# Optimization experiments

Measured on AMD Instinct MI355X. Metric: run time of the kernel, lower is better.

## Reference

```python
import jax, jax.numpy as jnp
import numpy as np

TEMPERATURE = 1.0
NUM_EXPERTS = 8


def setup_inputs() -> dict:
    key = jax.random.key(0)
    ks = jax.random.split(key, 7)
    B, S, H, E = 4, 4096, 1024, NUM_EXPERTS
    scale = 1.0 / np.sqrt(H)
    return {
        "hidden_states": jax.random.normal(ks[0], (B, S, H), dtype=jnp.float32),
        "w1": jax.random.normal(ks[1], (H, H // 2), dtype=jnp.float32) * scale,
        "b1": jax.random.normal(ks[2], (H // 2,), dtype=jnp.float32) * 0.01,
        "w2": jax.random.normal(ks[3], (H // 2, E), dtype=jnp.float32) * (1.0 / np.sqrt(H // 2)),
        "b2": jax.random.normal(ks[4], (E,), dtype=jnp.float32) * 0.01,
        "expert_W": jax.random.normal(ks[5], (E, H, H), dtype=jnp.float32) * scale,
        "expert_b": jax.random.normal(ks[6], (E, H), dtype=jnp.float32) * 0.01,
    }


def reference(hidden_states, w1, b1, w2, b2, expert_W, expert_b):
    # Router MLP: Linear(H, H//2) -> ReLU -> Linear(H//2, E)  (dropout inactive at eval)
    h = jax.nn.relu(jnp.einsum("bsh,hm->bsm", hidden_states, w1) + b1)
    routing_scores = (jnp.einsum("bsm,me->bse", h, w2) + b2) / TEMPERATURE
    expert_probs = jax.nn.softmax(routing_scores, axis=-1)
    # top-1 routing (topk with k=1 == argmax of probs)
    top_idx = jnp.argmax(expert_probs, axis=-1)  # [B, S]
    onehot = jax.nn.one_hot(top_idx, NUM_EXPERTS, dtype=hidden_states.dtype)  # [B, S, E]

    # _apply_expert_routing: for each expert, masked input -> dense transform -> masked accumulate
    routed = jnp.zeros_like(hidden_states)
    for e in range(NUM_EXPERTS):
        mask = onehot[..., e:e + 1]  # [B, S, 1]
        expert_out = jnp.einsum("bsh,hd->bsd", hidden_states * mask, expert_W[e]) + expert_b[e]
        routed = routed + expert_out * mask
    return routed
```

## Files before the change

### kernel.cpp

```cpp
#include <hip/hip_runtime.h>

#define NTOK 16384
#define HDIM 1024
#define MDIM 512
#define NEXP 8
#define CHUNK 128
#define MAXCHUNK 136
#define RCAP 4096
#define DELTA 0.02f
#define LSTR 72

#define G1_NWG ((MDIM / 128) * (NTOK / 128))
#define EG_NWG (8 * MAXCHUNK)

#define PREP_CVT 8192
#define PREP_W1 128
#define PREP_EW 2048
#define PREP_TOTAL (PREP_CVT + PREP_W1 + PREP_EW + 1)

typedef __bf16 bf16x8 __attribute__((ext_vector_type(8)));
typedef float floatx4 __attribute__((ext_vector_type(4)));

__device__ __forceinline__ void gll16(const void* g, void* l) {
  __builtin_amdgcn_global_load_lds(
      (const __attribute__((address_space(1))) void*)g,
      (__attribute__((address_space(3))) void*)l, 16, 0, 0);
}

__global__ __launch_bounds__(256) void prep(
    const float* __restrict__ hs, __bf16* __restrict__ hs_bf,
    const float* __restrict__ w1, __bf16* __restrict__ w1t,
    const float* __restrict__ eW, __bf16* __restrict__ eWt,
    int* __restrict__ ctrl, int* __restrict__ fillm1)
{
  __shared__ __align__(16) __bf16 T[64 * LSTR];
  const int bid = blockIdx.x;
  const int t = threadIdx.x;

  if (bid < PREP_CVT) {
    const size_t i = ((size_t)bid * 256 + t) * 8;
    float4 a = *(const float4*)&hs[i];
    float4 b = *(const float4*)&hs[i + 4];
    bf16x8 o;
    o[0] = (__bf16)a.x; o[1] = (__bf16)a.y; o[2] = (__bf16)a.z; o[3] = (__bf16)a.w;
    o[4] = (__bf16)b.x; o[5] = (__bf16)b.y; o[6] = (__bf16)b.z; o[7] = (__bf16)b.w;
    *(bf16x8*)&hs_bf[i] = o;
    return;
  }

  if (bid < PREP_CVT + PREP_W1 + PREP_EW) {
    int idx = bid - PREP_CVT;
    const float* S; __bf16* D; int K, C, k0, c0;
    if (idx < PREP_W1) {
      K = HDIM; C = MDIM;
      k0 = (idx & 15) * 64; c0 = (idx >> 4) * 64;
      S = w1; D = w1t;
    } else {
      idx -= PREP_W1;
      K = HDIM; C = HDIM;
      const int b = idx >> 8, r = idx & 255;
      k0 = (r & 15) * 64; c0 = (r >> 4) * 64;
      S = eW + (size_t)b * K * C; D = eWt + (size_t)b * K * C;
    }
    {
      const int rr = t >> 2, cc = (t & 3) * 16;
      const float* p = S + (size_t)(k0 + rr) * C + c0 + cc;
      float4 v0 = *(const float4*)&p[0];
      float4 v1 = *(const float4*)&p[4];
      float4 v2 = *(const float4*)&p[8];
      float4 v3 = *(const float4*)&p[12];
      float vv[16] = {v0.x, v0.y, v0.z, v0.w, v1.x, v1.y, v1.z, v1.w,
                      v2.x, v2.y, v2.z, v2.w, v3.x, v3.y, v3.z, v3.w};
#pragma unroll
      for (int j = 0; j < 16; ++j) T[(cc + j) * LSTR + rr] = (__bf16)vv[j];
    }
    __syncthreads();
    {
      const int c = t >> 2, kk = (t & 3) * 16;
      __bf16* q = D + (size_t)(c0 + c) * K + k0 + kk;
      *(float4*)&q[0] = *(const float4*)&T[c * LSTR + kk];
      *(float4*)&q[8] = *(const float4*)&T[c * LSTR + kk + 8];
    }
    return;
  }

  if (t < 32) ctrl[t] = 0;
  const int n = RCAP + MAXCHUNK * CHUNK;
  for (int i = t; i < n; i += 256) fillm1[i] = -1;
}

__global__ __launch_bounds__(256) void gemm1_score(
    const __bf16* __restrict__ A,
    const __bf16* __restrict__ Bt,
    const float* __restrict__ bias,
    const float* __restrict__ w2,
    float* __restrict__ scores_part)
{
  __shared__ __align__(16) __bf16 As[2 * 128 * 64];
  __shared__ __align__(16) __bf16 Bs[2 * 128 * 64];

  const int tid = threadIdx.x;
  const int swz = (blockIdx.x & 7) * (G1_NWG / 8) + (blockIdx.x >> 3);
  const int rowBlk = swz >> 2;
  const int cb = swz & 3;
  const int row0 = rowBlk * 128, col0 = cb * 128;
  const int wave = tid >> 6, lane = tid & 63;
  const int lrow8 = lane >> 3;
  const int gchunk = (lane & 7) ^ lrow8;
  const int wr = (wave >> 1) * 64, wc = (wave & 1) * 64;
  const int lrow = lane & 15, quad = lane >> 4;

  const __bf16 *pa[4], *pb[4];
#pragma unroll
  for (int p = 0; p < 4; ++p) {
    const int rb = wave * 8 + p * 32;
    pa[p] = A + (size_t)(row0 + rb + lrow8) * HDIM + gchunk * 8;
    pb[p] = Bt + (size_t)(col0 + rb + lrow8) * HDIM + gchunk * 8;
  }

  floatx4 acc[4][4];
#pragma unroll
  for (int i = 0; i < 4; ++i)
#pragma unroll
    for (int j = 0; j < 4; ++j) acc[i][j] = (floatx4){0.f, 0.f, 0.f, 0.f};

#pragma unroll
  for (int p = 0; p < 4; ++p) {
    const int rb = wave * 8 + p * 32;
    gll16(pa[p], &As[rb * 64]);
    gll16(pb[p], &Bs[rb * 64]);
  }
  __syncthreads();

  int cur = 0;
  for (int t = 0; t < HDIM / 64; ++t) {
    const int nxt = cur ^ 1;
    if (t + 1 < HDIM / 64) {
      const int koff = (t + 1) * 64;
#pragma unroll
      for (int p = 0; p < 4; ++p) {
        const int rb = wave * 8 + p * 32;
        gll16(pa[p] + koff, &As[nxt * 8192 + rb * 64]);
        gll16(pb[p] + koff, &Bs[nxt * 8192 + rb * 64]);
      }
    }
    const __bf16* Ab = &As[cur * 8192];
    const __bf16* Bb = &Bs[cur * 8192];
#pragma unroll
    for (int kh = 0; kh < 2; ++kh) {
      bf16x8 a[4], b[4];
#pragma unroll
      for (int i = 0; i < 4; ++i)
        a[i] = *(const bf16x8*)&Ab[(wr + i * 16 + lrow) * 64 +
                                   (((kh * 4 + quad) ^ (lrow & 7)) * 8)];
#pragma unroll
      for (int j = 0; j < 4; ++j)
        b[j] = *(const bf16x8*)&Bb[(wc + j * 16 + lrow) * 64 +
                                   (((kh * 4 + quad) ^ (lrow & 7)) * 8)];
#pragma unroll
      for (int i = 0; i < 4; ++i)
#pragma unroll
        for (int j = 0; j < 4; ++j)
          acc[i][j] = __builtin_amdgcn_mfma_f32_16x16x32_bf16(a[i], b[j], acc[i][j], 0, 0, 0);
    }
    __syncthreads();
    cur = nxt;
  }

  float* w2s = (float*)As;
  float* sblk = (float*)Bs;
  *(float4*)&w2s[tid * 4] = *(const float4*)&w2[col0 * 8 + tid * 4];
  __syncthreads();

  float bj[4];
  float4 wja[4], wjb[4];
#pragma unroll
  for (int j = 0; j < 4; ++j) {
    const int cl = wc + j * 16 + lrow;
    bj[j] = bias[col0 + cl];
    wja[j] = *(const float4*)&w2s[cl * 8];
    wjb[j] = *(const float4*)&w2s[cl * 8 + 4];
  }

#pragma unroll
  for (int i = 0; i < 4; ++i) {
#pragma unroll
    for (int r = 0; r < 4; ++r) {
      float4 sA = {0, 0, 0, 0}, sB = {0, 0, 0, 0};
#pragma unroll
      for (int j = 0; j < 4; ++j) {
        float h = fmaxf(acc[i][j][r] + bj[j], 0.f);
        sA.x += h * wja[j].x; sA.y += h * wja[j].y;
        sA.z += h * wja[j].z; sA.w += h * wja[j].w;
        sB.x += h * wjb[j].x; sB.y += h * wjb[j].y;
        sB.z += h * wjb[j].z; sB.w += h * wjb[j].w;
      }
#pragma unroll
      for (int m = 1; m <= 8; m <<= 1) {
        sA.x += __shfl_xor(sA.x, m, 64); sA.y += __shfl_xor(sA.y, m, 64);
        sA.z += __shfl_xor(sA.z, m, 64); sA.w += __shfl_xor(sA.w, m, 64);
        sB.x += __shfl_xor(sB.x, m, 64); sB.y += __shfl_xor(sB.y, m, 64);
        sB.z += __shfl_xor(sB.z, m, 64); sB.w += __shfl_xor(sB.w, m, 64);
      }
      if (lrow == 0) {
        const int rloc = wr + i * 16 + quad * 4 + r;
        *(float4*)&sblk[((wave & 1) * 128 + rloc) * 8] = sA;
        *(float4*)&sblk[((wave & 1) * 128 + rloc) * 8 + 4] = sB;
      }
    }
  }
  __syncthreads();
  {
    const int r = tid >> 1, e4 = (tid & 1) * 4;
    float4 v0 = *(const float4*)&sblk[r * 8 + e4];
    float4 v1 = *(const float4*)&sblk[(128 + r) * 8 + e4];
    float4 o = {v0.x + v1.x, v0.y + v1.y, v0.z + v1.z, v0.w + v1.w};
    *(float4*)&scores_part[((size_t)cb * NTOK + row0 + r) * 8 + e4] = o;
  }
}

__global__ __launch_bounds__(256) void routing_argmax(
    const float* __restrict__ scores_part, const float* __restrict__ b2,
    int* __restrict__ top_idx, int* __restrict__ risky_n,
    int* __restrict__ risky, int* __restrict__ counts)
{
  __shared__ int rbuf[256];
  __shared__ int lc[NEXP];
  __shared__ int rcnt, rbase;
  if (threadIdx.x == 0) rcnt = 0;
  if (threadIdx.x < NEXP) lc[threadIdx.x] = 0;
  __syncthreads();

  const int t = blockIdx.x * 256 + threadIdx.x;
  float4 sa = {0, 0, 0, 0}, sb = {0, 0, 0, 0};
#pragma unroll
  for (int c = 0; c < 4; ++c) {
    float4 va = *(const float4*)&scores_part[((size_t)c * NTOK + t) * 8];
    float4 vb = *(const float4*)&scores_part[((size_t)c * NTOK + t) * 8 + 4];
    sa.x += va.x; sa.y += va.y; sa.z += va.z; sa.w += va.w;
    sb.x += vb.x; sb.y += vb.y; sb.z += vb.z; sb.w += vb.w;
  }
  float s[8] = {sa.x + b2[0], sa.y + b2[1], sa.z + b2[2], sa.w + b2[3],
                sb.x + b2[4], sb.y + b2[5], sb.z + b2[6], sb.w + b2[7]};
  float best = s[0], second = -1e30f;
  int bi = 0;
#pragma unroll
  for (int e = 1; e < 8; ++e) {
    if (s[e] > best) { second = best; best = s[e]; bi = e; }
    else if (s[e] > second) second = s[e];
  }
  top_idx[t] = bi;
  atomicAdd(&lc[bi], 1);
  if (best - second < DELTA) rbuf[atomicAdd(&rcnt, 1)] = t;
  __syncthreads();
  if (threadIdx.x == 0 && rcnt > 0) rbase = atomicAdd(risky_n, rcnt);
  if (threadIdx.x < NEXP) atomicAdd(&counts[threadIdx.x], lc[threadIdx.x]);
  __syncthreads();
  if ((int)threadIdx.x < rcnt) {
    int slot = rbase + threadIdx.x;
    if (slot < RCAP) risky[slot] = rbuf[threadIdx.x];
  }
}

__global__ __launch_bounds__(256) void gemm1_fix_v2(
    const float* __restrict__ A, const float* __restrict__ W,
    const float* __restrict__ bias, const int* __restrict__ risky,
    float* __restrict__ hfix)
{
  __shared__ float As[32][33];
  __shared__ float Bs[32][64];
  __shared__ int toks[32];

  const int tid = threadIdx.x;
  if (tid < 32) toks[tid] = risky[blockIdx.y * 32 + tid];
  __syncthreads();
  if (toks[0] < 0) return;

  const int col0 = blockIdx.x * 64;
  const int tx = tid & 15, ty = tid >> 4;
  float acc0[4] = {0, 0, 0, 0}, acc1[4] = {0, 0, 0, 0};

  const int sr = tid >> 3;
  const int lo = tid & 7;
  const int sc8 = lo * 8;
  const int tokS = toks[sr];
  const float* pa = (tokS >= 0) ? A + (size_t)tokS * HDIM : A;

  for (int k0 = 0; k0 < HDIM; k0 += 32) {
    float4 av = make_float4(0, 0, 0, 0);
    if (tokS >= 0) av = *(const float4*)&pa[k0 + (lo & 3) * 4 + (lo >> 2) * 16];
    float4 b0 = *(const float4*)&W[(size_t)(k0 + sr) * MDIM + col0 + sc8];
    float4 b1v = *(const float4*)&W[(size_t)(k0 + sr) * MDIM + col0 + sc8 + 4];
    const int kk = (lo & 3) * 4 + (lo >> 2) * 16;
    As[kk + 0][sr] = av.x; As[kk + 1][sr] = av.y;
    As[kk + 2][sr] = av.z; As[kk + 3][sr] = av.w;
    *(float4*)&Bs[sr][sc8] = b0;
    *(float4*)&Bs[sr][sc8 + 4] = b1v;
    __syncthreads();

#pragma unroll
    for (int k = 0; k < 32; ++k) {
      float a0 = As[k][ty], a1 = As[k][ty + 16];
      float4 bv = *(const float4*)&Bs[k][tx * 4];
      acc0[0] = fmaf(a0, bv.x, acc0[0]); acc0[1] = fmaf(a0, bv.y, acc0[1]);
      acc0[2] = fmaf(a0, bv.z, acc0[2]); acc0[3] = fmaf(a0, bv.w, acc0[3]);
      acc1[0] = fmaf(a1, bv.x, acc1[0]); acc1[1] = fmaf(a1, bv.y, acc1[1]);
      acc1[2] = fmaf(a1, bv.z, acc1[2]); acc1[3] = fmaf(a1, bv.w, acc1[3]);
    }
    __syncthreads();
  }

  const int c = col0 + tx * 4;
  const int i0 = blockIdx.y * 32 + ty, i1 = blockIdx.y * 32 + ty + 16;
  if (toks[ty] >= 0) {
    float4 v;
    v.x = fmaxf(acc0[0] + bias[c + 0], 0.f); v.y = fmaxf(acc0[1] + bias[c + 1], 0.f);
    v.z = fmaxf(acc0[2] + bias[c + 2], 0.f); v.w = fmaxf(acc0[3] + bias[c + 3], 0.f);
    *(float4*)&hfix[(size_t)i0 * MDIM + c] = v;
  }
  if (toks[ty + 16] >= 0) {
    float4 v;
    v.x = fmaxf(acc1[0] + bias[c + 0], 0.f); v.y = fmaxf(acc1[1] + bias[c + 1], 0.f);
    v.z = fmaxf(acc1[2] + bias[c + 2], 0.f); v.w = fmaxf(acc1[3] + bias[c + 3], 0.f);
    *(float4*)&hfix[(size_t)i1 * MDIM + c] = v;
  }
}

__global__ __launch_bounds__(256) void rescore_fix(
    const float* __restrict__ hfix, const float* __restrict__ w2,
    const float* __restrict__ b2, const int* __restrict__ risky,
    int* __restrict__ top_idx, int* __restrict__ counts)
{
  const int idx = blockIdx.x * 32 + (threadIdx.x >> 3);
  const int l8 = threadIdx.x & 7;
  const int t = risky[idx];

  float s[8] = {0, 0, 0, 0, 0, 0, 0, 0};
  if (t >= 0) {
    const float* hrow = hfix + (size_t)idx * MDIM;
    for (int k = l8; k < MDIM; k += 8) {
      float hv = hrow[k];
      float4 wa = *(const float4*)&w2[k * 8];
      float4 wb = *(const float4*)&w2[k * 8 + 4];
      s[0] += hv * wa.x; s[1] += hv * wa.y; s[2] += hv * wa.z; s[3] += hv * wa.w;
      s[4] += hv * wb.x; s[5] += hv * wb.y; s[6] += hv * wb.z; s[7] += hv * wb.w;
    }
  }
#pragma unroll
  for (int off = 4; off > 0; off >>= 1)
#pragma unroll
    for (int e = 0; e < 8; ++e) s[e] += __shfl_xor(s[e], off, 64);

  if (l8 == 0 && t >= 0) {
    float best = s[0] + b2[0];
    int bi = 0;
#pragma unroll
    for (int e = 1; e < 8; ++e) {
      float v = s[e] + b2[e];
      if (v > best) { best = v; bi = e; }
    }
    const int old = top_idx[t];
    if (bi != old) {
      top_idx[t] = bi;
      atomicSub(&counts[old], 1);
      atomicAdd(&counts[bi], 1);
    }
  }
}

__global__ __launch_bounds__(256) void scatter_tokens(
    const int* __restrict__ top_idx, const int* __restrict__ counts,
    int* __restrict__ cursor, int* __restrict__ sorted)
{
  __shared__ int lc[NEXP], lbase[NEXP], off_s[NEXP];
  if (threadIdx.x < NEXP) lc[threadIdx.x] = 0;
  if (threadIdx.x == 0) {
    int off = 0;
    for (int e = 0; e < NEXP; ++e) {
      off_s[e] = off;
      off += ((counts[e] + CHUNK - 1) / CHUNK) * CHUNK;
    }
  }
  __syncthreads();
  const int t = blockIdx.x * 256 + threadIdx.x;
  const int e = top_idx[t];
  const int r = atomicAdd(&lc[e], 1);
  __syncthreads();
  if (threadIdx.x < NEXP)
    lbase[threadIdx.x] = atomicAdd(&cursor[threadIdx.x], lc[threadIdx.x]);
  __syncthreads();
  sorted[off_s[e] + lbase[e] + r] = t;
}

__global__ __launch_bounds__(256) void expert_gemm_v6(
    const __bf16* __restrict__ A,
    const __bf16* __restrict__ Wt,
    const float* __restrict__ Eb,
    const int* __restrict__ sorted,
    const int* __restrict__ top_idx,
    float* __restrict__ Out)
{
  __shared__ __align__(16) __bf16 As[2 * 128 * 64];
  __shared__ __align__(16) __bf16 Bs[2 * 128 * 64];
  __shared__ int toks[CHUNK];

  const int tid = threadIdx.x;
  const int swz = (blockIdx.x & 7) * (EG_NWG / 8) + (blockIdx.x >> 3);
  const int chunkIdx = swz >> 3;
  const int cb = swz & 7;
  if (tid < CHUNK) toks[tid] = sorted[(size_t)chunkIdx * CHUNK + tid];
  __syncthreads();
  if (toks[0] < 0) return;

  const int e = top_idx[toks[0]];
  const int col0 = cb * 128;
  const int wave = tid >> 6, lane = tid & 63;
  const int lrow8 = lane >> 3;
  const int gchunk = (lane & 7) ^ lrow8;
  const int wr = (wave >> 1) * 64, wc = (wave & 1) * 64;
  const int lrow = lane & 15, quad = lane >> 4;

  const __bf16 *pa[4], *pb[4];
#pragma unroll
  for (int p = 0; p < 4; ++p) {
    const int rb = wave * 8 + p * 32;
    const int tk = toks[rb + lrow8];
    pa[p] = A + (size_t)(tk < 0 ? 0 : tk) * HDIM + gchunk * 8;
    pb[p] = Wt + ((size_t)e * HDIM + col0 + rb + lrow8) * HDIM + gchunk * 8;
  }

  floatx4 acc[4][4];
#pragma unroll
  for (int i = 0; i < 4; ++i)
#pragma unroll
    for (int j = 0; j < 4; ++j) acc[i][j] = (floatx4){0.f, 0.f, 0.f, 0.f};

#pragma unroll
  for (int p = 0; p < 4; ++p) {
    const int rb = wave * 8 + p * 32;
    gll16(pa[p], &As[rb * 64]);
    gll16(pb[p], &Bs[rb * 64]);
  }
  __syncthreads();

  int cur = 0;
  for (int t = 0; t < HDIM / 64; ++t) {
    const int nxt = cur ^ 1;
    if (t + 1 < HDIM / 64) {
      const int koff = (t + 1) * 64;
#pragma unroll
      for (int p = 0; p < 4; ++p) {
        const int rb = wave * 8 + p * 32;
        gll16(pa[p] + koff, &As[nxt * 8192 + rb * 64]);
        gll16(pb[p] + koff, &Bs[nxt * 8192 + rb * 64]);
      }
    }
    const __bf16* Ab = &As[cur * 8192];
    const __bf16* Bb = &Bs[cur * 8192];
#pragma unroll
    for (int kh = 0; kh < 2; ++kh) {
      bf16x8 a[4], b[4];
#pragma unroll
      for (int i = 0; i < 4; ++i)
        a[i] = *(const bf16x8*)&Ab[(wr + i * 16 + lrow) * 64 +
                                   (((kh * 4 + quad) ^ (lrow & 7)) * 8)];
#pragma unroll
      for (int j = 0; j < 4; ++j)
        b[j] = *(const bf16x8*)&Bb[(wc + j * 16 + lrow) * 64 +
                                   (((kh * 4 + quad) ^ (lrow & 7)) * 8)];
#pragma unroll
      for (int i = 0; i < 4; ++i)
#pragma unroll
        for (int j = 0; j < 4; ++j)
          acc[i][j] = __builtin_amdgcn_mfma_f32_16x16x32_bf16(a[i], b[j], acc[i][j], 0, 0, 0);
    }
    __syncthreads();
    cur = nxt;
  }

  const float* be = Eb + (size_t)e * HDIM + col0;
#pragma unroll
  for (int i = 0; i < 4; ++i)
#pragma unroll
    for (int r = 0; r < 4; ++r) {
      const int row = wr + i * 16 + quad * 4 + r;
      const int tok = toks[row];
      if (tok < 0) continue;
      float* po = Out + (size_t)tok * HDIM + col0;
#pragma unroll
      for (int j = 0; j < 4; ++j) {
        const int col = wc + j * 16 + lrow;
        po[col] = acc[i][j][r] + be[col];
      }
    }
}

extern "C" void kernel_launch(void* const* d_in, const int* in_sizes, int n_in,
                              void* d_out, int out_size, void* d_ws, size_t ws_size,
                              hipStream_t stream) {
  (void)in_sizes; (void)n_in; (void)out_size; (void)ws_size;

  const float* hs = (const float*)d_in[0];
  const float* w1 = (const float*)d_in[1];
  const float* b1 = (const float*)d_in[2];
  const float* w2 = (const float*)d_in[3];
  const float* b2 = (const float*)d_in[4];
  const float* eW = (const float*)d_in[5];
  const float* eb = (const float*)d_in[6];
  float* out = (float*)d_out;

  float* hfix = (float*)d_out;
  float* scores_part = hfix + (size_t)RCAP * MDIM;

  char* wsb = (char*)d_ws;
  int* top_idx = (int*)wsb;
  int* ctrl    = (int*)(wsb + 65536);
  int* counts  = ctrl;
  int* risky_n = ctrl + 8;
  int* cursor  = ctrl + 16;
  int* risky   = (int*)(wsb + 65792);
  int* sorted  = risky + RCAP;
  __bf16* hs_bf = (__bf16*)(wsb + 163840);
  __bf16* w1t   = (__bf16*)(wsb + 163840 + 33554432);
  __bf16* eWt   = (__bf16*)(wsb + 163840 + 33554432 + 1048576);

  prep<<<PREP_TOTAL, 256, 0, stream>>>(hs, hs_bf, w1, w1t, eW, eWt, ctrl, risky);
  gemm1_score<<<dim3(G1_NWG), 256, 0, stream>>>(hs_bf, w1t, b1, w2, scores_part);
  routing_argmax<<<NTOK / 256, 256, 0, stream>>>(scores_part, b2, top_idx, risky_n, risky, counts);
  gemm1_fix_v2<<<dim3(MDIM / 64, RCAP / 32), 256, 0, stream>>>(hs, w1, b1, risky, hfix);
  rescore_fix<<<RCAP / 32, 256, 0, stream>>>(hfix, w2, b2, risky, top_idx, counts);
  scatter_tokens<<<NTOK / 256, 256, 0, stream>>>(top_idx, counts, cursor, sorted);
  expert_gemm_v6<<<dim3(EG_NWG), 256, 0, stream>>>(hs_bf, eWt, eb, sorted, top_idx, out);
}
```

Before: 317.6 us.

## Fuse routing argmax and rescore into preceding GEMMs via last-block counters

Removes two small kernel launches (routing_argmax and rescore_fix) by folding their work into gemm1_score and gemm1_fix. Each producer block bumps an atomic ready counter, and the last block to finish a row block (or token group) does the argmax or rescore itself. This saves launch gaps and a pass over scores_part, at the cost of extra atomics, thread fences and a serialized tail inside the last-arriving blocks. The control region grows, so the ready counters are zeroed in prep and risky is moved to a new offset.

```diff
diff --git a/kernel.cpp b/kernel.cpp
--- a/kernel.cpp
+++ b/kernel.cpp
@@ -17,6 +17,8 @@
 #define PREP_W1 128
 #define PREP_EW 2048
 #define PREP_TOTAL (PREP_CVT + PREP_W1 + PREP_EW + 1)
+
+#define CTRL_INTS 288
 
 typedef __bf16 bf16x8 __attribute__((ext_vector_type(8)));
 typedef float floatx4 __attribute__((ext_vector_type(4)));
@@ -84,7 +86,7 @@
     return;
   }
 
-  if (t < 32) ctrl[t] = 0;
+  for (int i = t; i < CTRL_INTS; i += 256) ctrl[i] = 0;
   const int n = RCAP + MAXCHUNK * CHUNK;
   for (int i = t; i < n; i += 256) fillm1[i] = -1;
 }
@@ -94,10 +96,17 @@
     const __bf16* __restrict__ Bt,
     const float* __restrict__ bias,
     const float* __restrict__ w2,
-    float* __restrict__ scores_part)
+    float* __restrict__ scores_part,
+    const float* __restrict__ b2,
+    int* __restrict__ top_idx, int* __restrict__ risky_n,
+    int* __restrict__ risky, int* __restrict__ counts,
+    int* __restrict__ ready1)
 {
   __shared__ __align__(16) __bf16 As[2 * 128 * 64];
   __shared__ __align__(16) __bf16 Bs[2 * 128 * 64];
+  __shared__ int rbuf[128];
+  __shared__ int lc[NEXP];
+  __shared__ int rcnt, rbase, amlast;
 
   const int tid = threadIdx.x;
   const int swz = (blockIdx.x & 7) * (G1_NWG / 8) + (blockIdx.x >> 3);
@@ -217,59 +226,62 @@
     float4 o = {v0.x + v1.x, v0.y + v1.y, v0.z + v1.z, v0.w + v1.w};
     *(float4*)&scores_part[((size_t)cb * NTOK + row0 + r) * 8 + e4] = o;
   }
-}
-
-__global__ __launch_bounds__(256) void routing_argmax(
-    const float* __restrict__ scores_part, const float* __restrict__ b2,
-    int* __restrict__ top_idx, int* __restrict__ risky_n,
-    int* __restrict__ risky, int* __restrict__ counts)
-{
-  __shared__ int rbuf[256];
-  __shared__ int lc[NEXP];
-  __shared__ int rcnt, rbase;
-  if (threadIdx.x == 0) rcnt = 0;
-  if (threadIdx.x < NEXP) lc[threadIdx.x] = 0;
-  __syncthreads();
-
-  const int t = blockIdx.x * 256 + threadIdx.x;
-  float4 sa = {0, 0, 0, 0}, sb = {0, 0, 0, 0};
-#pragma unroll
-  for (int c = 0; c < 4; ++c) {
-    float4 va = *(const float4*)&scores_part[((size_t)c * NTOK + t) * 8];
-    float4 vb = *(const float4*)&scores_part[((size_t)c * NTOK + t) * 8 + 4];
-    sa.x += va.x; sa.y += va.y; sa.z += va.z; sa.w += va.w;
-    sb.x += vb.x; sb.y += vb.y; sb.z += vb.z; sb.w += vb.w;
-  }
-  float s[8] = {sa.x + b2[0], sa.y + b2[1], sa.z + b2[2], sa.w + b2[3],
-                sb.x + b2[4], sb.y + b2[5], sb.z + b2[6], sb.w + b2[7]};
-  float best = s[0], second = -1e30f;
-  int bi = 0;
-#pragma unroll
-  for (int e = 1; e < 8; ++e) {
-    if (s[e] > best) { second = best; best = s[e]; bi = e; }
-    else if (s[e] > second) second = s[e];
-  }
-  top_idx[t] = bi;
-  atomicAdd(&lc[bi], 1);
-  if (best - second < DELTA) rbuf[atomicAdd(&rcnt, 1)] = t;
-  __syncthreads();
-  if (threadIdx.x == 0 && rcnt > 0) rbase = atomicAdd(risky_n, rcnt);
-  if (threadIdx.x < NEXP) atomicAdd(&counts[threadIdx.x], lc[threadIdx.x]);
-  __syncthreads();
-  if ((int)threadIdx.x < rcnt) {
-    int slot = rbase + threadIdx.x;
-    if (slot < RCAP) risky[slot] = rbuf[threadIdx.x];
-  }
-}
-
-__global__ __launch_bounds__(256) void gemm1_fix_v2(
+
+  __threadfence();
+  if (tid == 0) {
+    amlast = (atomicAdd(&ready1[rowBlk], 1) == 3);
+    rcnt = 0;
+  }
+  if (tid < NEXP) lc[tid] = 0;
+  __syncthreads();
+  if (!amlast) return;
+  __threadfence();
+
+  if (tid < 128) {
+    const int tok = row0 + tid;
+    float4 sa = {0, 0, 0, 0}, sb = {0, 0, 0, 0};
+#pragma unroll
+    for (int c = 0; c < 4; ++c) {
+      float4 va = *(const float4*)&scores_part[((size_t)c * NTOK + tok) * 8];
+      float4 vb = *(const float4*)&scores_part[((size_t)c * NTOK + tok) * 8 + 4];
+      sa.x += va.x; sa.y += va.y; sa.z += va.z; sa.w += va.w;
+      sb.x += vb.x; sb.y += vb.y; sb.z += vb.z; sb.w += vb.w;
+    }
+    float s[8] = {sa.x + b2[0], sa.y + b2[1], sa.z + b2[2], sa.w + b2[3],
+                  sb.x + b2[4], sb.y + b2[5], sb.z + b2[6], sb.w + b2[7]};
+    float best = s[0], second = -1e30f;
+    int bi = 0;
+#pragma unroll
+    for (int e = 1; e < 8; ++e) {
+      if (s[e] > best) { second = best; best = s[e]; bi = e; }
+      else if (s[e] > second) second = s[e];
+    }
+    top_idx[tok] = bi;
+    atomicAdd(&lc[bi], 1);
+    if (best - second < DELTA) rbuf[atomicAdd(&rcnt, 1)] = tok;
+  }
+  __syncthreads();
+  if (tid == 0 && rcnt > 0) rbase = atomicAdd(risky_n, rcnt);
+  if (tid < NEXP) atomicAdd(&counts[tid], lc[tid]);
+  __syncthreads();
+  if ((int)tid < rcnt) {
+    int slot = rbase + tid;
+    if (slot < RCAP) risky[slot] = rbuf[tid];
+  }
+}
+
+__global__ __launch_bounds__(256) void gemm1_fix(
     const float* __restrict__ A, const float* __restrict__ W,
     const float* __restrict__ bias, const int* __restrict__ risky,
-    float* __restrict__ hfix)
+    float* __restrict__ hfix,
+    const float* __restrict__ w2, const float* __restrict__ b2,
+    int* __restrict__ top_idx, int* __restrict__ counts,
+    int* __restrict__ ready2)
 {
   __shared__ float As[32][33];
   __shared__ float Bs[32][64];
   __shared__ int toks[32];
+  __shared__ int amlast;
 
   const int tid = threadIdx.x;
   if (tid < 32) toks[tid] = risky[blockIdx.y * 32 + tid];
@@ -324,46 +336,48 @@
     v.z = fmaxf(acc1[2] + bias[c + 2], 0.f); v.w = fmaxf(acc1[3] + bias[c + 3], 0.f);
     *(float4*)&hfix[(size_t)i1 * MDIM + c] = v;
   }
-}
-
-__global__ __launch_bounds__(256) void rescore_fix(
-    const float* __restrict__ hfix, const float* __restrict__ w2,
-    const float* __restrict__ b2, const int* __restrict__ risky,
-    int* __restrict__ top_idx, int* __restrict__ counts)
-{
-  const int idx = blockIdx.x * 32 + (threadIdx.x >> 3);
-  const int l8 = threadIdx.x & 7;
-  const int t = risky[idx];
-
-  float s[8] = {0, 0, 0, 0, 0, 0, 0, 0};
-  if (t >= 0) {
-    const float* hrow = hfix + (size_t)idx * MDIM;
-    for (int k = l8; k < MDIM; k += 8) {
-      float hv = hrow[k];
-      float4 wa = *(const float4*)&w2[k * 8];
-      float4 wb = *(const float4*)&w2[k * 8 + 4];
-      s[0] += hv * wa.x; s[1] += hv * wa.y; s[2] += hv * wa.z; s[3] += hv * wa.w;
-      s[4] += hv * wb.x; s[5] += hv * wb.y; s[6] += hv * wb.z; s[7] += hv * wb.w;
-    }
-  }
-#pragma unroll
-  for (int off = 4; off > 0; off >>= 1)
-#pragma unroll
-    for (int e = 0; e < 8; ++e) s[e] += __shfl_xor(s[e], off, 64);
-
-  if (l8 == 0 && t >= 0) {
-    float best = s[0] + b2[0];
-    int bi = 0;
-#pragma unroll
-    for (int e = 1; e < 8; ++e) {
-      float v = s[e] + b2[e];
-      if (v > best) { best = v; bi = e; }
-    }
-    const int old = top_idx[t];
-    if (bi != old) {
-      top_idx[t] = bi;
-      atomicSub(&counts[old], 1);
-      atomicAdd(&counts[bi], 1);
+
+  __threadfence();
+  if (tid == 0) amlast = (atomicAdd(&ready2[blockIdx.y], 1) == 7);
+  __syncthreads();
+  if (!amlast) return;
+  __threadfence();
+
+  {
+    const int idx = blockIdx.y * 32 + (tid >> 3);
+    const int l8 = tid & 7;
+    const int t = toks[tid >> 3];
+
+    float s[8] = {0, 0, 0, 0, 0, 0, 0, 0};
+    if (t >= 0) {
+      const float* hrow = hfix + (size_t)idx * MDIM;
+      for (int k = l8; k < MDIM; k += 8) {
+        float hv = hrow[k];
+        float4 wa = *(const float4*)&w2[k * 8];
+        float4 wb = *(const float4*)&w2[k * 8 + 4];
+        s[0] += hv * wa.x; s[1] += hv * wa.y; s[2] += hv * wa.z; s[3] += hv * wa.w;
+        s[4] += hv * wb.x; s[5] += hv * wb.y; s[6] += hv * wb.z; s[7] += hv * wb.w;
+      }
+    }
+#pragma unroll
+    for (int off = 4; off > 0; off >>= 1)
+#pragma unroll
+      for (int e = 0; e < 8; ++e) s[e] += __shfl_xor(s[e], off, 64);
+
+    if (l8 == 0 && t >= 0) {
+      float best = s[0] + b2[0];
+      int bi = 0;
+#pragma unroll
+      for (int e = 1; e < 8; ++e) {
+        float v = s[e] + b2[e];
+        if (v > best) { best = v; bi = e; }
+      }
+      const int old = top_idx[t];
+      if (bi != old) {
+        top_idx[t] = bi;
+        atomicSub(&counts[old], 1);
+        atomicAdd(&counts[bi], 1);
+      }
     }
   }
 }
@@ -518,17 +532,22 @@
   int* counts  = ctrl;
   int* risky_n = ctrl + 8;
   int* cursor  = ctrl + 16;
-  int* risky   = (int*)(wsb + 65792);
+  int* ready1  = ctrl + 32;
+  int* ready2  = ctrl + 160;
+  int* risky   = (int*)(wsb + 66688);
   int* sorted  = risky + RCAP;
   __bf16* hs_bf = (__bf16*)(wsb + 163840);
   __bf16* w1t   = (__bf16*)(wsb + 163840 + 33554432);
   __bf16* eWt   = (__bf16*)(wsb + 163840 + 33554432 + 1048576);
 
   prep<<<PREP_TOTAL, 256, 0, stream>>>(hs, hs_bf, w1, w1t, eW, eWt, ctrl, risky);
-  gemm1_score<<<dim3(G1_NWG), 256, 0, stream>>>(hs_bf, w1t, b1, w2, scores_part);
-  routing_argmax<<<NTOK / 256, 256, 0, stream>>>(scores_part, b2, top_idx, risky_n, risky, counts);
-  gemm1_fix_v2<<<dim3(MDIM / 64, RCAP / 32), 256, 0, stream>>>(hs, w1, b1, risky, hfix);
-  rescore_fix<<<RCAP / 32, 256, 0, stream>>>(hfix, w2, b2, risky, top_idx, counts);
+  gemm1_score<<<dim3(G1_NWG), 256, 0, stream>>>(hs_bf, w1t, b1, w2, scores_part,
+                                                b2, top_idx, risky_n, risky,
+                                                counts, ready1);
+  gemm1_fix<<<dim3(MDIM / 64, RCAP / 32), 256, 0, stream>>>(hs, w1, b1, risky,
+                                                            hfix, w2, b2,
+                                                            top_idx, counts,
+                                                            ready2);
   scatter_tokens<<<NTOK / 256, 256, 0, stream>>>(top_idx, counts, cursor, sorted);
   expert_gemm_v6<<<dim3(EG_NWG), 256, 0, stream>>>(hs_bf, eWt, eb, sorted, top_idx, out);
 }
```

Result: slower. 374.0 us (+17.8%).
